# Kernel optimization log

Measured on AMD Instinct MI355X. Metric: run time of the kernel, lower is better.

## Reference

```python
import jax, jax.numpy as jnp
import numpy as np

BLOCK, HALO, HEADS = 8, 4, 4


def setup_inputs() -> dict:
    key = jax.random.key(0)
    ks = jax.random.split(key, 9)
    B, C, H, W = 8, 256, 64, 64
    inner = C  # heads * dim_head = 4 * 64
    d = inner // HEADS
    R = BLOCK + 2 * HALO  # 16
    s = 0.02
    return {
        "x": jax.random.normal(ks[0], (B, C, H, W), jnp.float32),
        "wq": jax.random.normal(ks[1], (inner, C), jnp.float32) * s,
        "wkv": jax.random.normal(ks[2], (2 * inner, C), jnp.float32) * s,
        "wo": jax.random.normal(ks[3], (C, inner), jnp.float32) * s,
        "bo": jax.random.normal(ks[4], (C,), jnp.float32) * s,
        "rel_h": jax.random.normal(ks[5], (2 * R - 1, d), jnp.float32) * (d ** -0.5),
        "rel_w": jax.random.normal(ks[6], (2 * R - 1, d), jnp.float32) * (d ** -0.5),
        "w_conv": jax.random.normal(ks[7], (4 * C, C), jnp.float32) * s,
        "b_conv": jax.random.normal(ks[8], (4 * C,), jnp.float32) * s,
    }


def reference(x, wq, wkv, wo, bo, rel_h, rel_w, w_conv, b_conv):
    B, C, H, W = x.shape
    bs, halo, heads = BLOCK, HALO, HEADS
    R = bs + 2 * halo
    inner = wq.shape[0]
    d = inner // heads
    nh, nw = H // bs, W // bs
    Nb = B * nh * nw

    # ---- HaloAttention ----
    # block queries: (B, C, nh, bs, nw, bs) -> (Nb, bs*bs, C)
    q_in = x.reshape(B, C, nh, bs, nw, bs).transpose(0, 2, 4, 3, 5, 1).reshape(Nb, bs * bs, C)
    # haloed K/V windows via overlapping gather (== F.unfold(kernel=R, stride=bs, pad=halo))
    xp = jnp.pad(x, ((0, 0), (0, 0), (halo, halo), (halo, halo)))
    ridx = (jnp.arange(nh) * bs)[:, None] + jnp.arange(R)[None]  # (nh, R)
    cidx = (jnp.arange(nw) * bs)[:, None] + jnp.arange(R)[None]  # (nw, R)
    win = xp[:, :, ridx][:, :, :, :, cidx]                       # (B, C, nh, R, nw, R)
    kv_in = win.transpose(0, 2, 4, 3, 5, 1).reshape(Nb, R * R, C)

    q = (q_in @ wq.T).reshape(Nb, bs * bs, heads, d).transpose(0, 2, 1, 3) * (d ** -0.5)
    kv = kv_in @ wkv.T
    k, v = jnp.split(kv, 2, axis=-1)
    k = k.reshape(Nb, R * R, heads, d).transpose(0, 2, 1, 3)
    v = v.reshape(Nb, R * R, heads, d).transpose(0, 2, 1, 3)

    sim = jnp.einsum('bhid,bhjd->bhij', q, k)  # (Nb, heads, bs*bs, R*R)

    # relative position logits (computed from the scaled q, as in the torch code)
    q5 = q.reshape(Nb, heads, bs, bs, d)
    rel_idx = jnp.arange(R)[None, :] - jnp.arange(bs)[:, None] + (R - 1)  # (bs, R)
    lw = jnp.einsum('bhxyd,yjd->bhxyj', q5, rel_w[rel_idx])  # over key col j
    lh = jnp.einsum('bhxyd,xid->bhxyi', q5, rel_h[rel_idx])  # over key row i
    sim = sim.reshape(Nb, heads, bs, bs, R, R) + lw[..., None, :] + lh[..., None]
    sim = sim.reshape(Nb, heads, bs * bs, R * R)

    # mask out padded halo positions
    m = jnp.pad(jnp.ones((H, W), bool), ((halo, halo), (halo, halo)))
    mwin = m[ridx][:, :, cidx].transpose(0, 2, 1, 3).reshape(nh * nw, R * R)
    mask = jnp.broadcast_to(mwin[None], (B, nh * nw, R * R)).reshape(Nb, 1, 1, R * R)
    sim = jnp.where(mask, sim, -jnp.finfo(sim.dtype).max)

    attn = jax.nn.softmax(sim, axis=-1)
    out = jnp.einsum('bhij,bhjd->bhid', attn, v)
    out = out.transpose(0, 2, 1, 3).reshape(Nb, bs * bs, inner)
    out = out @ wo.T + bo  # (Nb, bs*bs, C)
    y = out.reshape(B, nh, nw, bs, bs, C).transpose(0, 5, 1, 3, 2, 4).reshape(B, C, H, W)

    # ---- Conv2d(dim, 4*dim, 1) + PixelShuffle(2) ----
    y = jnp.einsum('bchw,oc->bohw', y, w_conv) + b_conv[None, :, None, None]
    Cn = y.shape[1] // 4
    y = y.reshape(B, Cn, 2, 2, H, W).transpose(0, 1, 4, 2, 5, 3).reshape(B, Cn, 2 * H, 2 * W)
    return y
```

## Files before the change

kernel.cpp:

```cpp
#include <hip/hip_runtime.h>

typedef unsigned short u16;
typedef unsigned int u32;
typedef __attribute__((ext_vector_type(8))) short short8;
typedef __attribute__((ext_vector_type(4))) float f32x4;

__device__ __forceinline__ float bf2f(u16 u){ union { u32 i; float f; } x; x.i = ((u32)u)<<16; return x.f; }
__device__ __forceinline__ u16 f2bf(float f){ union { float f; u32 i; } x; x.f = f; u32 r = x.i + 0x7fffu + ((x.i>>16)&1u); return (u16)(r>>16); }

#define MFMA16(a,b,c) __builtin_amdgcn_mfma_f32_16x16x32_bf16((a),(b),(c),0,0,0)

__device__ __forceinline__ uint4 ld8(const void* p, size_t off, int f32) {
  if (f32) {
    const float* fp = (const float*)p + off;
    float4 a = *(const float4*)fp;
    float4 b = *(const float4*)(fp + 4);
    uint4 o;
    o.x = (u32)f2bf(a.x) | ((u32)f2bf(a.y)<<16);
    o.y = (u32)f2bf(a.z) | ((u32)f2bf(a.w)<<16);
    o.z = (u32)f2bf(b.x) | ((u32)f2bf(b.y)<<16);
    o.w = (u32)f2bf(b.z) | ((u32)f2bf(b.w)<<16);
    return o;
  }
  return *(const uint4*)((const u16*)p + off);
}
__device__ __forceinline__ uint2 ld4(const void* p, size_t off, int f32) {
  if (f32) {
    const float* fp = (const float*)p + off;
    float4 a = *(const float4*)fp;
    uint2 o;
    o.x = (u32)f2bf(a.x) | ((u32)f2bf(a.y)<<16);
    o.y = (u32)f2bf(a.z) | ((u32)f2bf(a.w)<<16);
    return o;
  }
  return *(const uint2*)((const u16*)p + off);
}
__device__ __forceinline__ float ldsc(const void* p, size_t off, int f32) {
  if (f32) return ((const float*)p)[off];
  return bf2f(((const u16*)p)[off]);
}

__global__ __launch_bounds__(256) void k_detect(const u32* __restrict__ x, int* __restrict__ flag)
{
  __shared__ int cnt;
  if (threadIdx.x == 0) cnt = 0;
  __syncthreads();
  int c = 0;
  #pragma unroll
  for (int i = 0; i < 32; ++i) {
    u32 w = x[threadIdx.x*32 + i];
    u32 e = (w >> 7) & 0xFFu;
    c += (e == 0u || (e >= 96u && e <= 143u)) ? 1 : 0;
  }
  atomicAdd(&cnt, c);
  __syncthreads();
  if (threadIdx.x == 0) *flag = (cnt < 4915) ? 1 : 0;
}

__global__ __launch_bounds__(256) void k_fuse_w(
  const u32* __restrict__ x,
  const void* __restrict__ wo, const void* __restrict__ wconv,
  const void* __restrict__ bo, const void* __restrict__ bconv,
  u16* __restrict__ F, float* __restrict__ bfus, int* __restrict__ flagp)
{
  __shared__ int cnt;
  __shared__ __align__(16) u16 WC[16*256];
  __shared__ __align__(16) u16 WO[32*128];
  __shared__ float bred[16][17];
  const int t = threadIdx.x;
  if (t == 0) cnt = 0;
  __syncthreads();
  {
    int c = 0;
    #pragma unroll
    for (int i=0;i<8;++i) {
      u32 w = x[t*8+i];
      u32 e = (w>>7)&0xFFu;
      c += (e==0u || (e>=96u && e<=143u)) ? 1 : 0;
    }
    atomicAdd(&cnt, c);
  }
  __syncthreads();
  const int f32 = (cnt < 1229) ? 1 : 0;
  if (blockIdx.x == 0 && blockIdx.y == 0 && t == 0) *flagp = f32;
  const int o0 = blockIdx.x*16, c0 = blockIdx.y*128;
  {
    int row = t>>4, ch = (t&15)*16;
    *(uint4*)&WC[row*256+ch]     = ld8(wconv, (size_t)(o0+row)*256 + ch, f32);
    *(uint4*)&WC[row*256+ch+8]   = ld8(wconv, (size_t)(o0+row)*256 + ch + 8, f32);
  }
  float acc[8] = {};
  const int ty = t>>4, tx = t&15;
  for (int jc=0;jc<8;++jc) {
    __syncthreads();
    {
      int jr = t>>3, cc = (t&7)*16;
      *(uint4*)&WO[jr*128+cc]   = ld8(wo, (size_t)(jc*32+jr)*256 + c0 + cc, f32);
      *(uint4*)&WO[jr*128+cc+8] = ld8(wo, (size_t)(jc*32+jr)*256 + c0 + cc + 8, f32);
    }
    __syncthreads();
    #pragma unroll 4
    for (int jj=0;jj<32;++jj) {
      float wv = bf2f(WC[ty*256 + jc*32 + jj]);
      short8 w8 = *(const short8*)&WO[jj*128 + tx*8];
      #pragma unroll
      for (int i=0;i<8;++i) acc[i] += wv * bf2f((u16)w8[i]);
    }
  }
  {
    u32 pw[4];
    #pragma unroll
    for (int j=0;j<4;++j) pw[j] = (u32)f2bf(acc[2*j]) | ((u32)f2bf(acc[2*j+1])<<16);
    *(uint4*)&F[(size_t)(o0+ty)*256 + c0 + tx*8] = *(uint4*)pw;
  }
  if (blockIdx.y == 0) {
    float s = 0.0f;
    #pragma unroll 4
    for (int j=tx*16; j<tx*16+16; ++j) s += bf2f(WC[ty*256+j]) * ldsc(bo, j, f32);
    bred[ty][tx] = s;
  }
  __syncthreads();
  if (blockIdx.y == 0 && t < 16) {
    float s = 0.0f;
    #pragma unroll
    for (int p=0;p<16;++p) s += bred[t][p];
    bfus[o0+t] = s + ldsc(bconv, o0+t, f32);
  }
}

__global__ __launch_bounds__(256) void k_transpose(const void* __restrict__ x, u16* __restrict__ xt,
                                                   const int* __restrict__ flagp)
{
  __shared__ int sflag;
  __shared__ __align__(16) u16 tile[64][68];
  if (threadIdx.x == 0) sflag = *flagp;
  __syncthreads();
  const int f32 = sflag;
  const int p0 = blockIdx.x*64, c0 = blockIdx.y*64, b = blockIdx.z;
  const int t = threadIdx.x;
  const size_t xbo = ((size_t)(b*256 + c0))*4096 + p0;
  #pragma unroll
  for (int pass=0; pass<4; ++pass) {
    int cl = pass*16 + (t>>4);
    int pl = (t&15)*4;
    uint2 v = ld4(x, xbo + (size_t)cl*4096 + pl, f32);
    *(uint2*)&tile[cl][pl] = v;
  }
  __syncthreads();
  u16* xtb = xt + ((size_t)b*4096 + p0)*256 + c0;
  #pragma unroll
  for (int pass=0; pass<4; ++pass) {
    int pl = pass*16 + (t>>4);
    int cl = (t&15)*4;
    unsigned int lo = (unsigned int)tile[cl][pl]   | ((unsigned int)tile[cl+1][pl]<<16);
    unsigned int hi = (unsigned int)tile[cl+2][pl] | ((unsigned int)tile[cl+3][pl]<<16);
    uint2 o; o.x = lo; o.y = hi;
    *(uint2*)(xtb + (size_t)pl*256 + cl) = o;
  }
}

__global__ __launch_bounds__(256) void k_gemm_bt(
  const u16* __restrict__ A, int lda,
  const void* __restrict__ Bt0, const void* __restrict__ Bt1, int nsplit,
  const void* __restrict__ bias,
  void* __restrict__ C, int M, int N, int K,
  float s_lo, float s_hi, int shuffle, int internalB,
  const int* __restrict__ flagp)
{
  __shared__ int sflag;
  __shared__ __align__(16) char smem[18432];
  if (threadIdx.x == 0) sflag = *flagp;
  __syncthreads();
  const int f32 = sflag;
  const int bf = internalB ? 0 : f32;
  const int biasf = internalB ? 1 : f32;
  const int m0 = blockIdx.x*128, n0 = blockIdx.y*128;
  const void* Bs; int boff;
  if (Bt1 && n0 >= nsplit) { Bs = Bt1; boff = n0 - nsplit; } else { Bs = Bt0; boff = n0; }
  const int t = threadIdx.x, lane = t & 63, wv = t >> 6;
  const int wm = (wv & 1)*64, wn = (wv >> 1)*64;
  const int lm = lane & 15, lq = lane >> 4;
  f32x4 acc[4][4] = {};

  const u16* arow[4];
  size_t brow[4];
  #pragma unroll
  for (int i=0;i<4;++i) {
    arow[i] = A + (size_t)(m0 + wm + i*16 + lm)*lda + lq*8;
    brow[i] = (size_t)(boff + wn + i*16 + lm)*K + lq*8;
  }

  #pragma unroll 2
  for (int k0 = 0; k0 < K; k0 += 32) {
    short8 af[4], bfr[4];
    #pragma unroll
    for (int i=0;i<4;++i) af[i] = *(const short8*)(arow[i] + k0);
    #pragma unroll
    for (int i=0;i<4;++i) { uint4 v = ld8(Bs, brow[i] + k0, bf); bfr[i] = *(const short8*)&v; }
    #pragma unroll
    for (int mt=0;mt<4;++mt)
      #pragma unroll
      for (int nt=0;nt<4;++nt)
        acc[mt][nt] = MFMA16(af[mt], bfr[nt], acc[mt][nt]);
  }

  if (!shuffle) {
    u16* eh = (u16*)smem;
    #pragma unroll
    for (int c=0;c<2;++c) {
      __syncthreads();
      if ((wv>>1) == c) {
        #pragma unroll
        for (int nt=0;nt<4;++nt) {
          int col = n0 + c*64 + nt*16 + lm;
          float sc = (col < nsplit) ? s_lo : s_hi;
          float bv = bias ? ldsc(bias, col, biasf) : 0.0f;
          #pragma unroll
          for (int mt=0;mt<4;++mt)
            #pragma unroll
            for (int r=0;r<4;++r) {
              int row = wm + mt*16 + lq*4 + r;
              eh[row*72 + nt*16 + lm] = f2bf(acc[mt][nt][r]*sc + bv);
            }
        }
      }
      __syncthreads();
      {
        int row = t >> 1, off = (t & 1)*32;
        const uint4* s = (const uint4*)&eh[row*72 + off];
        uint4 v0 = s[0], v1 = s[1], v2 = s[2], v3 = s[3];
        uint4* dp = (uint4*)((u16*)C + (size_t)(m0+row)*N + n0 + c*64 + off);
        dp[0]=v0; dp[1]=v1; dp[2]=v2; dp[3]=v3;
      }
    }
  } else {
    float* ef = (float*)smem;
    const int b = m0 >> 12;
    const int hh0 = (m0 & 4095) >> 6;
    #pragma unroll
    for (int c=0;c<4;++c) {
      __syncthreads();
      if ((wv>>1) == (c>>1)) {
        #pragma unroll
        for (int nt2=0;nt2<2;++nt2) {
          int nt = (c&1)*2 + nt2;
          int col = n0 + wn + nt*16 + lm;
          float bv = bias ? ldsc(bias, col, biasf) : 0.0f;
          int col_rel = nt2*16 + lm;
          int cn_rel = col_rel >> 2, rr = (col_rel >> 1) & 1, ss = col_rel & 1;
          #pragma unroll
          for (int mt=0;mt<4;++mt)
            #pragma unroll
            for (int r=0;r<4;++r) {
              int row = wm + mt*16 + lq*4 + r;
              int orow = cn_rel*4 + (row>>6)*2 + rr;
              int ow   = (row & 63)*2 + ss;
              ef[orow*134 + ow] = acc[mt][nt][r]*s_hi + bv;
            }
        }
      }
      __syncthreads();
      {
        int orow = t >> 3, seg = t & 7;
        int cn_rel = orow >> 2, oh_rel = orow & 3;
        int cn = ((n0 + c*32) >> 2) + cn_rel;
        size_t obase = (((size_t)(b*256 + cn))*128 + hh0*2 + oh_rel)*128 + seg*16;
        const float4* s = (const float4*)&ef[orow*134 + seg*16];
        float4 v0 = s[0], v1 = s[1], v2 = s[2], v3 = s[3];
        if (f32) {
          float4* dp = (float4*)((float*)C + obase);
          dp[0]=v0; dp[1]=v1; dp[2]=v2; dp[3]=v3;
        } else {
          float vv[16];
          *(float4*)&vv[0]=v0; *(float4*)&vv[4]=v1; *(float4*)&vv[8]=v2; *(float4*)&vv[12]=v3;
          u32 pw[8];
          #pragma unroll
          for (int j=0;j<8;++j) pw[j] = (u32)f2bf(vv[2*j]) | ((u32)f2bf(vv[2*j+1])<<16);
          u16* dp = (u16*)C + obase;
          *(uint4*)dp       = *(uint4*)&pw[0];
          *(uint4*)(dp + 8) = *(uint4*)&pw[4];
        }
      }
    }
  }
}

#define MASKVAL (-30000.0f)
__global__ __launch_bounds__(256) void k_halo_attn(
  const u16* __restrict__ qkv,
  const void* __restrict__ relh, const void* __restrict__ relw,
  u16* __restrict__ aout, int ostride,
  const int* __restrict__ flagp)
{
  __shared__ int sflag;
  __shared__ __align__(16) u16 Qs[64*72];
  __shared__ __align__(16) u16 KP[128*72];
  __shared__ __align__(16) u16 Vt[64*136];
  __shared__ __align__(16) u16 Gw[64*32];
  __shared__ __align__(16) u16 Gh[64*32];
  if (threadIdx.x == 0) sflag = *flagp;
  __syncthreads();
  const int f32 = sflag;

  const int blk = blockIdx.x, head = blockIdx.y;
  const int bb = blk >> 6, by = (blk >> 3) & 7, bx = blk & 7;
  const int h0 = by*8, w0 = bx*8;
  const int t = threadIdx.x, lane = t & 63, wv = t >> 6;
  const int lm = lane & 15, lq = lane >> 4;
  const size_t pixbase = (size_t)bb * 4096;
  const float LOG2E = 1.4426950408889634f;

  #pragma unroll
  for (int i=0;i<2;++i) {
    int u = t + i*256;
    int row = u >> 3, ch = (u & 7)*8;
    int qx = row >> 3, qy = row & 7;
    size_t p = pixbase + (size_t)(h0+qx)*64 + (w0+qy);
    *(uint4*)&Qs[row*72 + ch] = *(const uint4*)(qkv + p*768 + head*64 + ch);
  }
  {
    u16* RW = KP; u16* RH = KP + 2048;
    if (t < 248) {
      *(uint4*)&RW[t*8] = ld8(relw, (size_t)t*8, f32);
      *(uint4*)&RH[t*8] = ld8(relh, (size_t)t*8, f32);
    } else {
      uint4 z; z.x=z.y=z.z=z.w=0;
      int o = 1984 + (t-248)*8;
      *(uint4*)&RW[o] = z;
      *(uint4*)&RH[o] = z;
    }
  }
  __syncthreads();
  {
    const u16* RW = KP; const u16* RH = KP + 2048;
    f32x4 agw[2] = {}, agh[2] = {};
    #pragma unroll
    for (int ks=0;ks<2;++ks) {
      short8 aq = *(const short8*)&Qs[(wv*16 + lm)*72 + ks*32 + lq*8];
      #pragma unroll
      for (int nt=0;nt<2;++nt) {
        short8 bw = *(const short8*)&RW[(nt*16 + lm)*64 + ks*32 + lq*8];
        short8 bh = *(const short8*)&RH[(nt*16 + lm)*64 + ks*32 + lq*8];
        agw[nt] = MFMA16(aq, bw, agw[nt]);
        agh[nt] = MFMA16(aq, bh, agh[nt]);
      }
    }
    #pragma unroll
    for (int nt=0;nt<2;++nt)
      #pragma unroll
      for (int r=0;r<4;++r) {
        int m = wv*16 + lq*4 + r, c = nt*16 + lm;
        Gw[m*32 + c] = f2bf(agw[nt][r]);
        Gh[m*32 + c] = f2bf(agh[nt][r]);
      }
  }
  __syncthreads();

  float m_run[4], l_run[4];
  #pragma unroll
  for (int r=0;r<4;++r){ m_run[r] = MASKVAL; l_run[r] = 0.0f; }
  f32x4 acc_o[4] = {};

  for (int tile=0; tile<2; ++tile) {
    #pragma unroll
    for (int i=0;i<4;++i) {
      int u = t + i*256;
      int kl = u >> 3, ch = (u & 7)*8;
      int ki = tile*8 + (kl >> 4), kj = kl & 15;
      int hk = h0 - 4 + ki, wk = w0 - 4 + kj;
      uint4 v; v.x=v.y=v.z=v.w=0;
      if ((unsigned)hk < 64u && (unsigned)wk < 64u) {
        size_t p = pixbase + (size_t)hk*64 + wk;
        v = *(const uint4*)(qkv + p*768 + 256 + head*64 + ch);
      }
      *(uint4*)&KP[kl*72 + ch] = v;
    }
    {
      int kl = t & 127, db = (t >> 7)*32;
      int ki = tile*8 + (kl >> 4), kj = kl & 15;
      int hk = h0 - 4 + ki, wk = w0 - 4 + kj;
      bool ok = ((unsigned)hk < 64u) && ((unsigned)wk < 64u);
      size_t p = pixbase + (size_t)hk*64 + wk;
      const u16* vp = qkv + p*768 + 512 + head*64 + db;
      #pragma unroll
      for (int c=0;c<4;++c) {
        union { uint4 v; u16 s[8]; } uu;
        uu.v.x=uu.v.y=uu.v.z=uu.v.w=0;
        if (ok) uu.v = *(const uint4*)(vp + c*8);
        #pragma unroll
        for (int jj=0;jj<8;++jj) Vt[(db + c*8 + jj)*136 + kl] = uu.s[jj];
      }
    }
    __syncthreads();
    f32x4 as[8] = {};
    #pragma unroll
    for (int ks=0;ks<2;++ks) {
      short8 aq = *(const short8*)&Qs[(wv*16 + lm)*72 + ks*32 + lq*8];
      #pragma unroll
      for (int nt=0;nt<8;++nt) {
        short8 bk = *(const short8*)&KP[(nt*16 + lm)*72 + ks*32 + lq*8];
        as[nt] = MFMA16(aq, bk, as[nt]);
      }
    }
    __syncthreads();
    #pragma unroll
    for (int r=0;r<4;++r) {
      int m = wv*16 + lq*4 + r;
      int qx = m >> 3, qy = m & 7;
      float vals[8]; float rowmax = MASKVAL;
      #pragma unroll
      for (int nt=0;nt<8;++nt) {
        int ki = tile*8 + nt;
        int hk = h0 - 4 + ki, wk = w0 - 4 + lm;
        float v = as[nt][r]
                + bf2f(Gw[m*32 + (lm - qy + 15)])
                + bf2f(Gh[m*32 + (ki - qx + 15)]);
        if (!((unsigned)hk < 64u && (unsigned)wk < 64u)) v = MASKVAL;
        vals[nt] = v;
        rowmax = fmaxf(rowmax, v);
      }
      #pragma unroll
      for (int s=1;s<16;s<<=1) rowmax = fmaxf(rowmax, __shfl_xor(rowmax, s, 64));
      float mnew = fmaxf(m_run[r], rowmax);
      float alpha = exp2f((m_run[r] - mnew)*LOG2E);
      float rs = 0.0f;
      #pragma unroll
      for (int nt=0;nt<8;++nt) {
        float e = exp2f((vals[nt] - mnew)*LOG2E);
        rs += e;
        KP[m*136 + nt*16 + lm] = f2bf(e);
      }
      #pragma unroll
      for (int s=1;s<16;s<<=1) rs += __shfl_xor(rs, s, 64);
      l_run[r] = l_run[r]*alpha + rs;
      m_run[r] = mnew;
      #pragma unroll
      for (int nt=0;nt<4;++nt) acc_o[nt][r] *= alpha;
    }
    __syncthreads();
    #pragma unroll
    for (int ks=0;ks<4;++ks) {
      short8 ap = *(const short8*)&KP[(wv*16 + lm)*136 + ks*32 + lq*8];
      #pragma unroll
      for (int nt=0;nt<4;++nt) {
        short8 bv = *(const short8*)&Vt[(nt*16 + lm)*136 + ks*32 + lq*8];
        acc_o[nt] = MFMA16(ap, bv, acc_o[nt]);
      }
    }
    __syncthreads();
  }
  #pragma unroll
  for (int nt=0;nt<4;++nt)
    #pragma unroll
    for (int r=0;r<4;++r) {
      int m = wv*16 + lq*4 + r;
      int qx = m >> 3, qy = m & 7;
      size_t p = pixbase + (size_t)(h0+qx)*64 + (w0+qy);
      aout[p*(size_t)ostride + head*64 + nt*16 + lm] = f2bf(acc_o[nt][r]/l_run[r]);
    }
}

extern "C" void kernel_launch(void* const* d_in, const int* in_sizes, int n_in,
                              void* d_out, int out_size, void* d_ws, size_t ws_size,
                              hipStream_t stream)
{
  const void* x     = d_in[0];
  const void* wq    = d_in[1];
  const void* wkv   = d_in[2];
  const void* wo    = d_in[3];
  const void* bo    = d_in[4];
  const void* relh  = d_in[5];
  const void* relw  = d_in[6];
  const void* wconv = d_in[7];
  const void* bconv = d_in[8];

  int*  flag = (int*)d_ws;
  u16*  base = (u16*)d_out;
  u16*  qkv  = base;
  u16*  xt   = base + 25165824;

  const size_t WS_FUSED = 4096 + 524288 + 4096 + 16777216;

  if (ws_size >= WS_FUSED) {
    u16*   Wf   = (u16*)((char*)d_ws + 4096);
    float* bfus = (float*)((char*)d_ws + 4096 + 524288);
    u16*   aout = (u16*)((char*)d_ws + 4096 + 524288 + 4096);
    k_fuse_w<<<dim3(64,2), 256, 0, stream>>>((const u32*)x, wo, wconv, bo, bconv,
                                             Wf, bfus, flag);
    k_transpose<<<dim3(64,4,8), 256, 0, stream>>>(x, xt, flag);
    k_gemm_bt<<<dim3(256,6), 256, 0, stream>>>(xt, 256, wq, wkv, 256, nullptr,
                                               qkv, 32768, 768, 256, 0.125f, 1.0f, 0, 0, flag);
    k_halo_attn<<<dim3(512,4), 256, 0, stream>>>(qkv, relh, relw, aout, 256, flag);
    k_gemm_bt<<<dim3(256,8), 256, 0, stream>>>(aout, 256, Wf, nullptr, 0, bfus,
                                               d_out, 32768, 1024, 256, 1.0f, 1.0f, 1, 1, flag);
  } else {
    u16* y2 = (u16*)((char*)d_ws + 4096);
    k_detect<<<1, 256, 0, stream>>>((const u32*)x, flag);
    k_transpose<<<dim3(64,4,8), 256, 0, stream>>>(x, xt, flag);
    k_gemm_bt<<<dim3(256,6), 256, 0, stream>>>(xt, 256, wq, wkv, 256, nullptr,
                                               qkv, 32768, 768, 256, 0.125f, 1.0f, 0, 0, flag);
    k_halo_attn<<<dim3(512,4), 256, 0, stream>>>(qkv, relh, relw, qkv, 768, flag);
    k_gemm_bt<<<dim3(256,2), 256, 0, stream>>>(qkv, 768, wo, nullptr, 0, bo,
                                               y2, 32768, 256, 256, 1.0f, 1.0f, 0, 0, flag);
    k_gemm_bt<<<dim3(256,8), 256, 0, stream>>>(y2, 256, wconv, nullptr, 0, bconv,
                                               d_out, 32768, 1024, 256, 1.0f, 1.0f, 1, 0, flag);
  }
}
```

Before: 407.5 us.

## Fuse NCHW-to-token transpose into QKV GEMM via LDS staging of x

Drops the separate k_transpose kernel. The QKV GEMM now reads x straight from NCHW layout, converts it to bf16, and transposes each 128x32 A tile through LDS before the MFMAs. The wq/wkv weights are pre-converted to a packed bf16 Wqkv buffer inside k_fuse_w using an extra grid row. This removes one full activation write and read round trip, but the GEMM k-loop gains two barriers per step and LDS stores with a 40-element row stride that may cause bank conflicts.

```diff
diff --git a/kernel.cpp b/kernel.cpp
--- a/kernel.cpp
+++ b/kernel.cpp
@@ -59,9 +59,11 @@
 
 __global__ __launch_bounds__(256) void k_fuse_w(
   const u32* __restrict__ x,
+  const void* __restrict__ wq, const void* __restrict__ wkv,
   const void* __restrict__ wo, const void* __restrict__ wconv,
   const void* __restrict__ bo, const void* __restrict__ bconv,
-  u16* __restrict__ F, float* __restrict__ bfus, int* __restrict__ flagp)
+  u16* __restrict__ F, float* __restrict__ bfus, u16* __restrict__ Wqkv,
+  int* __restrict__ flagp)
 {
   __shared__ int cnt;
   __shared__ __align__(16) u16 WC[16*256];
@@ -83,6 +85,23 @@
   __syncthreads();
   const int f32 = (cnt < 1229) ? 1 : 0;
   if (blockIdx.x == 0 && blockIdx.y == 0 && t == 0) *flagp = f32;
+
+  if (blockIdx.y == 2) {
+    int rbase = blockIdx.x * 12;
+    #pragma unroll
+    for (int p=0;p<2;++p) {
+      int rr = p*8 + (t>>5);
+      int cg = (t&31)*8;
+      if (rr < 12) {
+        int row = rbase + rr;
+        uint4 w = (row < 256) ? ld8(wq, (size_t)row*256 + cg, f32)
+                              : ld8(wkv, (size_t)(row-256)*256 + cg, f32);
+        *(uint4*)&Wqkv[(size_t)row*256 + cg] = w;
+      }
+    }
+    return;
+  }
+
   const int o0 = blockIdx.x*16, c0 = blockIdx.y*128;
   {
     int row = t>>4, ch = (t&15)*16;
@@ -160,11 +179,11 @@
 }
 
 __global__ __launch_bounds__(256) void k_gemm_bt(
-  const u16* __restrict__ A, int lda,
+  const void* __restrict__ A, int lda,
   const void* __restrict__ Bt0, const void* __restrict__ Bt1, int nsplit,
   const void* __restrict__ bias,
   void* __restrict__ C, int M, int N, int K,
-  float s_lo, float s_hi, int shuffle, int internalB,
+  float s_lo, float s_hi, int shuffle, int internalB, int xpose,
   const int* __restrict__ flagp)
 {
   __shared__ int sflag;
@@ -182,26 +201,66 @@
   const int lm = lane & 15, lq = lane >> 4;
   f32x4 acc[4][4] = {};
 
-  const u16* arow[4];
-  size_t brow[4];
-  #pragma unroll
-  for (int i=0;i<4;++i) {
-    arow[i] = A + (size_t)(m0 + wm + i*16 + lm)*lda + lq*8;
-    brow[i] = (size_t)(boff + wn + i*16 + lm)*K + lq*8;
-  }
-
-  #pragma unroll 2
-  for (int k0 = 0; k0 < K; k0 += 32) {
-    short8 af[4], bfr[4];
-    #pragma unroll
-    for (int i=0;i<4;++i) af[i] = *(const short8*)(arow[i] + k0);
-    #pragma unroll
-    for (int i=0;i<4;++i) { uint4 v = ld8(Bs, brow[i] + k0, bf); bfr[i] = *(const short8*)&v; }
-    #pragma unroll
-    for (int mt=0;mt<4;++mt)
-      #pragma unroll
-      for (int nt=0;nt<4;++nt)
-        acc[mt][nt] = MFMA16(af[mt], bfr[nt], acc[mt][nt]);
+  if (xpose) {
+    u16* Als = (u16*)smem;
+    const int bb = m0 >> 12, px0 = m0 & 4095;
+    const int ch = t & 31, pg = t >> 5;
+    const u16* Bq = (const u16*)Bs;
+    for (int k0 = 0; k0 < K; k0 += 32) {
+      if (k0) __syncthreads();
+      {
+        size_t xo = ((size_t)(bb*256 + k0 + ch))*4096 + px0 + pg*16;
+        u16 v[16];
+        if (f32) {
+          const float* fp = (const float*)A + xo;
+          float4 q0 = *(const float4*)fp,     q1 = *(const float4*)(fp+4);
+          float4 q2 = *(const float4*)(fp+8), q3 = *(const float4*)(fp+12);
+          v[0]=f2bf(q0.x); v[1]=f2bf(q0.y); v[2]=f2bf(q0.z); v[3]=f2bf(q0.w);
+          v[4]=f2bf(q1.x); v[5]=f2bf(q1.y); v[6]=f2bf(q1.z); v[7]=f2bf(q1.w);
+          v[8]=f2bf(q2.x); v[9]=f2bf(q2.y); v[10]=f2bf(q2.z); v[11]=f2bf(q2.w);
+          v[12]=f2bf(q3.x); v[13]=f2bf(q3.y); v[14]=f2bf(q3.z); v[15]=f2bf(q3.w);
+        } else {
+          const u16* hp = (const u16*)A + xo;
+          *(uint4*)&v[0] = *(const uint4*)hp;
+          *(uint4*)&v[8] = *(const uint4*)(hp+8);
+        }
+        #pragma unroll
+        for (int j=0;j<16;++j) Als[(pg*16 + j)*40 + ch] = v[j];
+      }
+      __syncthreads();
+      short8 af[4], bfr[4];
+      #pragma unroll
+      for (int i=0;i<4;++i) af[i] = *(const short8*)&Als[(wm + i*16 + lm)*40 + lq*8];
+      #pragma unroll
+      for (int i=0;i<4;++i) bfr[i] = *(const short8*)(Bq + (size_t)(boff + wn + i*16 + lm)*K + k0 + lq*8);
+      #pragma unroll
+      for (int mt=0;mt<4;++mt)
+        #pragma unroll
+        for (int nt=0;nt<4;++nt)
+          acc[mt][nt] = MFMA16(af[mt], bfr[nt], acc[mt][nt]);
+    }
+  } else {
+    const u16* Au = (const u16*)A;
+    const u16* arow[4];
+    size_t brow[4];
+    #pragma unroll
+    for (int i=0;i<4;++i) {
+      arow[i] = Au + (size_t)(m0 + wm + i*16 + lm)*lda + lq*8;
+      brow[i] = (size_t)(boff + wn + i*16 + lm)*K + lq*8;
+    }
+    #pragma unroll 2
+    for (int k0 = 0; k0 < K; k0 += 32) {
+      short8 af[4], bfr[4];
+      #pragma unroll
+      for (int i=0;i<4;++i) af[i] = *(const short8*)(arow[i] + k0);
+      #pragma unroll
+      for (int i=0;i<4;++i) { uint4 v = ld8(Bs, brow[i] + k0, bf); bfr[i] = *(const short8*)&v; }
+      #pragma unroll
+      for (int mt=0;mt<4;++mt)
+        #pragma unroll
+        for (int nt=0;nt<4;++nt)
+          acc[mt][nt] = MFMA16(af[mt], bfr[nt], acc[mt][nt]);
+    }
   }
 
   if (!shuffle) {
@@ -485,24 +544,24 @@
     u16*   Wf   = (u16*)((char*)d_ws + 4096);
     float* bfus = (float*)((char*)d_ws + 4096 + 524288);
     u16*   aout = (u16*)((char*)d_ws + 4096 + 524288 + 4096);
-    k_fuse_w<<<dim3(64,2), 256, 0, stream>>>((const u32*)x, wo, wconv, bo, bconv,
-                                             Wf, bfus, flag);
-    k_transpose<<<dim3(64,4,8), 256, 0, stream>>>(x, xt, flag);
-    k_gemm_bt<<<dim3(256,6), 256, 0, stream>>>(xt, 256, wq, wkv, 256, nullptr,
-                                               qkv, 32768, 768, 256, 0.125f, 1.0f, 0, 0, flag);
+    u16*   Wqkv = aout;
+    k_fuse_w<<<dim3(64,3), 256, 0, stream>>>((const u32*)x, wq, wkv, wo, wconv, bo, bconv,
+                                             Wf, bfus, Wqkv, flag);
+    k_gemm_bt<<<dim3(256,6), 256, 0, stream>>>(x, 0, Wqkv, nullptr, 256, nullptr,
+                                               qkv, 32768, 768, 256, 0.125f, 1.0f, 0, 1, 1, flag);
     k_halo_attn<<<dim3(512,4), 256, 0, stream>>>(qkv, relh, relw, aout, 256, flag);
     k_gemm_bt<<<dim3(256,8), 256, 0, stream>>>(aout, 256, Wf, nullptr, 0, bfus,
-                                               d_out, 32768, 1024, 256, 1.0f, 1.0f, 1, 1, flag);
+                                               d_out, 32768, 1024, 256, 1.0f, 1.0f, 1, 1, 0, flag);
   } else {
     u16* y2 = (u16*)((char*)d_ws + 4096);
     k_detect<<<1, 256, 0, stream>>>((const u32*)x, flag);
     k_transpose<<<dim3(64,4,8), 256, 0, stream>>>(x, xt, flag);
     k_gemm_bt<<<dim3(256,6), 256, 0, stream>>>(xt, 256, wq, wkv, 256, nullptr,
-                                               qkv, 32768, 768, 256, 0.125f, 1.0f, 0, 0, flag);
+                                               qkv, 32768, 768, 256, 0.125f, 1.0f, 0, 0, 0, flag);
     k_halo_attn<<<dim3(512,4), 256, 0, stream>>>(qkv, relh, relw, qkv, 768, flag);
     k_gemm_bt<<<dim3(256,2), 256, 0, stream>>>(qkv, 768, wo, nullptr, 0, bo,
-                                               y2, 32768, 256, 256, 1.0f, 1.0f, 0, 0, flag);
+                                               y2, 32768, 256, 256, 1.0f, 1.0f, 0, 0, 0, flag);
     k_gemm_bt<<<dim3(256,8), 256, 0, stream>>>(y2, 256, wconv, nullptr, 0, bconv,
-                                               d_out, 32768, 1024, 256, 1.0f, 1.0f, 1, 0, flag);
-  }
-}
+                                               d_out, 32768, 1024, 256, 1.0f, 1.0f, 1, 0, 0, flag);
+  }
+}
```

Measured after the change: 367.8 us. -9.8%, faster.
